# Kernel optimization log

Hardware: AMD Instinct MI355X
Metric: run time of the kernel (lower is better)

Reference implementation:

```python
import jax, jax.numpy as jnp
import numpy as np


def lstm(x, W, U, b):
    """Keras LSTM with activation='relu', recurrent_activation='sigmoid'.
    x: [B, S, E]; W: [E, 4u]; U: [u, 4u]; b: [4u]. Gate order i,f,c,o.
    Returns (all hidden states [B,S,u], last hidden [B,u])."""
    B = x.shape[0]
    u = U.shape[0]
    h0 = jnp.zeros((B, u), x.dtype)
    c0 = jnp.zeros((B, u), x.dtype)

    def step(carry, xt):
        h, c = carry
        z = xt @ W + h @ U + b
        i, f, g, o = jnp.split(z, 4, axis=-1)
        i = jax.nn.sigmoid(i)
        f = jax.nn.sigmoid(f)
        g = jax.nn.relu(g)          # candidate activation = relu
        o = jax.nn.sigmoid(o)
        c = f * c + i * g
        h = o * jax.nn.relu(c)      # output activation = relu
        return (h, c), h

    (hT, _), hs = jax.lax.scan(step, (h0, c0), jnp.swapaxes(x, 0, 1))
    return jnp.swapaxes(hs, 0, 1), hT


def setup_inputs() -> dict:
    key = jax.random.key(0)
    ks = iter(jax.random.split(key, 64))

    def W(*s):
        return jax.random.normal(next(ks), s, jnp.float32) * 0.05

    V = 32000
    inp = {
        "t": jax.random.randint(next(ks), (8, 16, 64), 0, V, jnp.int32),
        "p": jax.random.randint(next(ks), (8, 16, 512), 0, V, jnp.int32),
        "emb_t": W(V, 128),
        "emb_p": W(V, 256),
        # title LSTMs: 128 (return_seq) -> 64
        "tl0_W": W(128, 512), "tl0_U": W(128, 512), "tl0_b": jnp.zeros((512,), jnp.float32),
        "tl1_W": W(128, 256), "tl1_U": W(64, 256),  "tl1_b": jnp.zeros((256,), jnp.float32),
        # title dense: 128 relu, 64 relu, 32 linear
        "td0_W": W(64, 128),  "td0_b": jnp.zeros((128,), jnp.float32),
        "td1_W": W(128, 64),  "td1_b": jnp.zeros((64,), jnp.float32),
        "td2_W": W(64, 32),   "td2_b": jnp.zeros((32,), jnp.float32),
        # parag LSTMs: 256 (rs) -> 128 (rs) -> 64
        "pl0_W": W(256, 1024), "pl0_U": W(256, 1024), "pl0_b": jnp.zeros((1024,), jnp.float32),
        "pl1_W": W(256, 512),  "pl1_U": W(128, 512),  "pl1_b": jnp.zeros((512,), jnp.float32),
        "pl2_W": W(128, 256),  "pl2_U": W(64, 256),   "pl2_b": jnp.zeros((256,), jnp.float32),
        # parag dense: 128 relu, 64 relu, 32 linear
        "pd0_W": W(64, 128),  "pd0_b": jnp.zeros((128,), jnp.float32),
        "pd1_W": W(128, 64),  "pd1_b": jnp.zeros((64,), jnp.float32),
        "pd2_W": W(64, 32),   "pd2_b": jnp.zeros((32,), jnp.float32),
        # head: 256 relu, 128 relu, 64 relu, 32 sigmoid
        "L0_W": W(64, 256),  "L0_b": jnp.zeros((256,), jnp.float32),
        "L1_W": W(256, 128), "L1_b": jnp.zeros((128,), jnp.float32),
        "L2_W": W(128, 64),  "L2_b": jnp.zeros((64,), jnp.float32),
        "L3_W": W(64, 32),   "L3_b": jnp.zeros((32,), jnp.float32),
    }
    return inp


def reference(t, p, emb_t, emb_p,
              tl0_W, tl0_U, tl0_b, tl1_W, tl1_U, tl1_b,
              td0_W, td0_b, td1_W, td1_b, td2_W, td2_b,
              pl0_W, pl0_U, pl0_b, pl1_W, pl1_U, pl1_b, pl2_W, pl2_U, pl2_b,
              pd0_W, pd0_b, pd1_W, pd1_b, pd2_W, pd2_b,
              L0_W, L0_b, L1_W, L1_b, L2_W, L2_b, L3_W, L3_b):
    B, N, St = t.shape
    Sp = p.shape[2]

    # The original loops over B and map_fn over a singleton axis; the math is
    # identical to running the stacks on a flattened [B*N] recurrent batch.
    xt = emb_t[t.reshape(B * N, St)]              # [BN, St, 128]
    xt, _ = lstm(xt, tl0_W, tl0_U, tl0_b)         # [BN, St, 128]
    _, ht = lstm(xt, tl1_W, tl1_U, tl1_b)         # [BN, 64]
    ht = jax.nn.relu(ht @ td0_W + td0_b)
    ht = jax.nn.relu(ht @ td1_W + td1_b)
    ht = ht @ td2_W + td2_b                       # [BN, 32] (no activation)

    xp = emb_p[p.reshape(B * N, Sp)]              # [BN, Sp, 256]
    xp, _ = lstm(xp, pl0_W, pl0_U, pl0_b)
    xp, _ = lstm(xp, pl1_W, pl1_U, pl1_b)
    _, hp = lstm(xp, pl2_W, pl2_U, pl2_b)         # [BN, 64]
    hp = jax.nn.relu(hp @ pd0_W + pd0_b)
    hp = jax.nn.relu(hp @ pd1_W + pd1_b)
    hp = hp @ pd2_W + pd2_b                       # [BN, 32]

    feat = jnp.concatenate([ht, hp], axis=-1).reshape(B, N, 64)
    x = feat.mean(axis=1)                         # reduce_mean over axis=-2 (N)
    x = jax.nn.relu(x @ L0_W + L0_b)
    x = jax.nn.relu(x @ L1_W + L1_b)
    x = jax.nn.relu(x @ L2_W + L2_b)
    x = jax.nn.sigmoid(x @ L3_W + L3_b)           # [B, 32]
    return x
```

## Files before the change

### kernel.cpp

```cpp
#include <hip/hip_runtime.h>
#include <hip/hip_fp16.h>

typedef _Float16 f16;
typedef _Float16 f16x8 __attribute__((ext_vector_type(8)));
typedef float    f32x4 __attribute__((ext_vector_type(4)));
typedef unsigned short ushort;
typedef unsigned int uint;
typedef unsigned long long u64;

__device__ __forceinline__ float sigm(float x) { return 1.f / (1.f + __expf(-x)); }
__device__ __forceinline__ float reluf(float x) { return x > 0.f ? x : 0.f; }
__device__ __forceinline__ float h2f(ushort u) { return (float)__builtin_bit_cast(f16, u); }
__device__ __forceinline__ ushort f2h(float v) { return __builtin_bit_cast(ushort, (f16)v); }

#define LDRLX(p)    __hip_atomic_load((p), __ATOMIC_RELAXED, __HIP_MEMORY_SCOPE_AGENT)
#define STRLX(p, v) __hip_atomic_store((p), (v), __ATOMIC_RELAXED, __HIP_MEMORY_SCOPE_AGENT)
#define MFMA16(a, b, c) __builtin_amdgcn_mfma_f32_16x16x32_f16((a), (b), (c), 0, 0, 0)
#define LBAR() do { asm volatile("s_waitcnt lgkmcnt(0)" ::: "memory"); \
                    __builtin_amdgcn_s_barrier(); } while (0)

__device__ __forceinline__ void poll_all(uint* p, uint need, bool act) {
  bool done = !act;
  while (true) {
    if (!done) done = (LDRLX(p) >= need);
// ... 35 lines not shown
  if (id >= total) return;
  int j  = id & 7;
  int L  = (id >> 3) & 63;
  int r  = id >> 9;
  int kf = r & (KF - 1);
  int c  = r / KF;
  int k  = kf * 32 + ((L >> 4) * 8) + j;
  int n  = c * 16 + (L & 15);
  dst[id] = (f16)B[k * N + n];
}

template <int Sx, int K, int KF, int N, int NC, int MODE>
__global__ __launch_bounds__(256) void gemm_xw(const int* __restrict__ tok,
                                               const float* __restrict__ emb,
                                               const f16* __restrict__ Bsw,
                                               const float* __restrict__ bias,
                                               f16* __restrict__ X) {
  __shared__ int tokLds[64];
  __shared__ f16x8 bLds[8 * 64];
  const int tid = threadIdx.x;
  const int blk = blockIdx.x;
  const int g  = (MODE == 0) ? (blk >> 7) : (blk >> 4);
  const int t0 = (MODE == 0) ? ((blk & 127) * 4) : ((blk & 15) * 4);
  if (tid < 64) {
    int wv = tid >> 4, rho = tid & 15;
    tokLds[tid] = tok[(g * 16 + rho) * Sx + t0 + wv];
  }
  __syncthreads();
  const int wave = tid >> 6, lane = tid & 63;
  const int quad = lane >> 4, l16 = lane & 15;

  f16x8 a[KF];
  {
    const float* arow = emb + (long)tokLds[wave * 16 + l16] * K + quad * 8;
#pragma unroll
    for (int kf = 0; kf < KF; kf++) {
      float4 v0 = *(const float4*)(arow + kf * 32);
      float4 v1 = *(const float4*)(arow + kf * 32 + 4);
      f16x8 tv;
      tv[0] = (f16)v0.x; tv[1] = (f16)v0.y; tv[2] = (f16)v0.z; tv[3] = (f16)v0.w;
      tv[4] = (f16)v1.x; tv[5] = (f16)v1.y; tv[6] = (f16)v1.z; tv[7] = (f16)v1.w;
      a[kf] = tv;
    }
  }
  const int t = t0 + wave;
  const f16x8* Bfrag = (const f16x8*)Bsw;
  for (int c = 0; c < NC; c++) {
    for (int i = tid; i < KF * 64; i += 256) bLds[i] = Bfrag[c * KF * 64 + i];
    __syncthreads();
    f32x4 acc = {0.f, 0.f, 0.f, 0.f};
#pragma unroll
    for (int kf = 0; kf < KF; kf++)
      acc = MFMA16(a[kf], bLds[kf * 64 + lane], acc);
    const int col = c * 16 + l16;
    const float bc = bias[col];
    uint2 pk;
    pk.x = (uint)f2h(acc[0] + bc) | ((uint)f2h(acc[1] + bc) << 16);
    pk.y = (uint)f2h(acc[2] + bc) | ((uint)f2h(acc[3] + bc) << 16);
    size_t base;
    if (MODE == 0) {
      int gm = col >> 8, u = col & 255;
      base = (((size_t)(g * 512 + t) * 4 + gm) * 4096) + u * 16 + quad * 4;
    } else {
      int gm = col >> 7, u = col & 127;
      base = (((size_t)(g * 64 + t) * 4 + gm) * 2048) + u * 16 + quad * 4;
    }
    *(uint2*)(X + base) = pk;
    __syncthreads();
  }
}

struct RP {
  const f16 *xp2, *xt2;
  const f16 *U0f, *W1f, *U1f, *W2f, *U2f, *U0tf, *W1tf, *U1tf;
  const float *pl1_b, *pl2_b, *tl1_b;
  const float *pd0W, *pd0b, *pd1W, *pd1b, *pd2W, *pd2b;
  const float *td0W, *td0b, *td1W, *td1b, *td2W, *td2b;
  u64 *h0r, *h1r, *h0tr;
  uint *cnt;
  float* feat;
};

__global__ __launch_bounds__(256, 1) void recur_pipe(RP A) {
  __shared__ __align__(16) char smem[147968];
  const int tid = threadIdx.x;
  const int w = tid >> 6, lane = tid & 63;
  const int quad = lane >> 4, l16 = lane & 15;
  const int blk = blockIdx.x;
  const int role = blk >> 3, g = blk & 7;
  uint* mytag = A.cnt + (role * 8 + g) * 16;

  if (role < 4) {
    const int bb = role;
    f16* wlds = (f16*)smem;
    f16* hb   = (f16*)(smem + 131072);
    {
      const uint4* U0q = (const uint4*)A.U0f;
      uint4* wq = (uint4*)wlds;
      for (int idx = tid; idx < 8192; idx += 256) {
        int gm = idx >> 11, r = idx & 2047, wv = r >> 9, kf = (r >> 6) & 7, ln = r & 63;
        wq[idx] = U0q[((gm * 16 + 4 * bb + wv) * 8 + kf) * 64 + ln];
      }
    }
    for (int idx = tid; idx < 4224; idx += 256) hb[idx] = (f16)0.f;
    float c0[4] = {0.f, 0.f, 0.f, 0.f};
    u64* ringg = A.h0r + (size_t)g * 16384;
    int pp[3]; { int q = 0; for (int p = 0; p < 4; p++) if (p != bb) pp[q++] = p; }
    const uint2* xq2 = (const uint2*)A.xp2;
    const f16x8* wv8 = (const f16x8*)wlds;
    const int myu = 64 * bb + 16 * w + l16;
    const int ulq = 16 * ((tid >> 4) & 3) + (tid & 15);
    const int qd  = tid >> 6;
    uint* bpp = A.cnt;
    if (lane < 4) bpp = A.cnt + ((4 + lane) * 8 + g) * 16;
    __syncthreads();

    for (int t = 0; t < 512; t++) {
      uint2 xv[4];
      {
        size_t xb = ((size_t)(g * 512 + t) * 4) * 1024 + (size_t)myu * 4 + quad;
#pragma unroll
        for (int gm = 0; gm < 4; gm++) xv[gm] = xq2[xb + (size_t)gm * 1024];
      }
      {
        bool act = (lane < 4) && (t > 0) && ((t & 3) == 0);
        uint need = t > 4 ? (uint)(t - 4) : 0u;
        poll_all(bpp, need, act);
      }
      {
        const u64* slotb = ringg + (size_t)((t + 7) & 7) * 2048;
        const u64* ra[6]; uint nd[6]; u64 rv[6];
#pragma unroll
        for (int q = 0; q < 3; q++) {
          const u64* rb = slotb + pp[q] * 512 + 2 * tid;
          ra[q * 2] = rb; ra[q * 2 + 1] = rb + 1;
          nd[q * 2] = nd[q * 2 + 1] = (t > 0) ? (uint)t : 0u;
        }
        poll_recs<6>(ra, nd, rv);
        if (t > 0) {
          f16* dst = hb + (t & 1) * 4224;
#pragma unroll
          for (int q = 0; q < 3; q++)
#pragma unroll
            for (int j = 0; j < 2; j++) {
              uint pay = (uint)rv[q * 2 + j];
              int r0 = qd * 4 + 2 * j;
              dst[r0 * 264 + pp[q] * 64 + ulq]       = __builtin_bit_cast(f16, (ushort)pay);
              dst[(r0 + 1) * 264 + pp[q] * 64 + ulq] = __builtin_bit_cast(f16, (ushort)(pay >> 16));
            }
        }
      }
      LBAR();
      f16x8 af[8];
#pragma unroll
      for (int kf = 0; kf < 8; kf++)
        af[kf] = *(const f16x8*)&hb[(t & 1) * 4224 + l16 * 264 + kf * 32 + quad * 8];
      f32x4 z[4];
#pragma unroll
      for (int gm = 0; gm < 4; gm++) {
        f32x4 zz = {0.f, 0.f, 0.f, 0.f};
#pragma unroll
        for (int kf = 0; kf < 8; kf++)
          zz = MFMA16(af[kf], wv8[((gm * 4 + w) * 8 + kf) * 64 + lane], zz);
        z[gm] = zz;
      }
      u64 xs[4];
#pragma unroll
      for (int gm = 0; gm < 4; gm++) xs[gm] = ((u64)xv[gm].y << 32) | xv[gm].x;
      ushort hs[4];
      f16* wbuf = hb + ((t + 1) & 1) * 4224;
#pragma unroll
      for (int r = 0; r < 4; r++) {
        float gi = sigm(z[0][r] + h2f((ushort)(xs[0] >> (16 * r))));
        float ff = sigm(z[1][r] + h2f((ushort)(xs[1] >> (16 * r))));
        float gg = reluf(z[2][r] + h2f((ushort)(xs[2] >> (16 * r))));
        float oo = sigm(z[3][r] + h2f((ushort)(xs[3] >> (16 * r))));
        c0[r] = ff * c0[r] + gi * gg;
        hs[r] = f2h(oo * reluf(c0[r]));
        wbuf[(quad * 4 + r) * 264 + myu] = __builtin_bit_cast(f16, hs[r]);
      }
      {
        u64 tg = ((u64)(uint)(t + 1)) << 32;
        u64* wb = ringg + (size_t)(t & 7) * 2048 + bb * 512 +
                  quad * 128 + w * 32 + l16 * 2;
        str64(wb,     tg | (u64)((uint)hs[0] | ((uint)hs[1] << 16)));
        str64(wb + 1, tg | (u64)((uint)hs[2] | ((uint)hs[3] << 16)));
      }
    }
  } else if (role < 8) {
    const int bn = role - 4;
    f16* wlds = (f16*)smem;
    f16* h0c  = (f16*)(smem + 98304);
    f16* h1b  = (f16*)(smem + 106752);
    float* zL = (float*)(smem + 115456);
    {
      const uint4* W1q = (const uint4*)A.W1f;
      const uint4* U1q = (const uint4*)A.U1f;
      uint4* wq = (uint4*)wlds;
      for (int idx = tid; idx < 4096; idx += 256) {
        int gm = idx >> 10, r = idx & 1023, j2 = r >> 9, kf = (r >> 6) & 7, ln = r & 63;
        wq[idx] = W1q[((gm * 8 + bn * 2 + j2) * 8 + kf) * 64 + ln];
      }
      for (int idx = tid; idx < 2048; idx += 256) {
        int gm = idx >> 9, r = idx & 511, j2 = r >> 8, kf = (r >> 6) & 3, ln = r & 63;
        wq[4096 + idx] = U1q[((gm * 8 + bn * 2 + j2) * 4 + kf) * 64 + ln];
      }
    }
    for (int idx = tid; idx < 2176; idx += 256) h1b[idx] = (f16)0.f;
    float c1[2] = {0.f, 0.f};
    float bth[4];
    { int un = tid & 31; for (int gm = 0; gm < 4; gm++) bth[gm] = A.pl1_b[gm * 128 + 32 * bn + un]; }
    u64* h0rg = A.h0r + (size_t)g * 16384;
    u64* h1rg = A.h1r + (size_t)g * 8192;
    int pp[3]; { int q = 0; for (int p = 0; p < 4; p++) if (p != bn) pp[q++] = p; }
    const f16x8* wv8 = (const f16x8*)wlds;
    uint* bpp = A.cnt + (8 * 8 + g) * 16;
    __syncthreads();

    for (int t = 0; t < 512; t++) {
      {
        bool act = (lane == 0) && ((t & 3) == 0);
        uint need = t > 4 ? (uint)(t - 4) : 0u;
        poll_all(bpp, need, act);
      }
      const u64* ra[11]; uint nd[11]; u64 rv[11];
      {
        const u64* s0b = h0rg + (size_t)(t & 7) * 2048;
#pragma unroll
        for (int e = 0; e < 8; e++) { ra[e] = s0b + tid + 256 * e; nd[e] = (uint)(t + 1); }
        const u64* s1b = h1rg + (size_t)((t + 7) & 7) * 1024;
#pragma unroll
        for (int q = 0; q < 3; q++) { ra[8 + q] = s1b + pp[q] * 256 + tid; nd[8 + q] = (t > 0) ? (uint)t : 0u; }
      }
      poll_recs<11>(ra, nd, rv);
      {
#pragma unroll
        for (int e = 0; e < 8; e++) {
          int idx = tid + 256 * e;
          int bbq = idx >> 9, r = idx & 511;
          int jj = r & 1, l16c = (r >> 1) & 15, wc = (r >> 5) & 3, qdc = (r >> 7) & 3;
          int col = bbq * 64 + 16 * wc + l16c;
          int r0 = qdc * 4 + 2 * jj;
          uint pay = (uint)rv[e];
          h0c[r0 * 264 + col]       = __builtin_bit_cast(f16, (ushort)pay);
          h0c[(r0 + 1) * 264 + col] = __builtin_bit_cast(f16, (ushort)(pay >> 16));
        }
        if (t > 0) {
          f16* dst = h1b + (t & 1) * 2176;
          int sqc = tid >> 5, unc = tid & 31;
#pragma unroll
          for (int q = 0; q < 3; q++) {
            uint pay = (uint)rv[8 + q];
            dst[sqc * 136 + pp[q] * 32 + unc]       = __builtin_bit_cast(f16, (ushort)pay);
            dst[(sqc + 8) * 136 + pp[q] * 32 + unc] = __builtin_bit_cast(f16, (ushort)(pay >> 16));
          }
        }
      }
      LBAR();
      if (tid == 0) STRLX(mytag, (uint)(t + 1));
      f16x8 af0[8], af1[4];
#pragma unroll
      for (int kf = 0; kf < 8; kf++)
        af0[kf] = *(const f16x8*)&h0c[l16 * 264 + kf * 32 + quad * 8];
#pragma unroll
      for (int kf = 0; kf < 4; kf++)
        af1[kf] = *(const f16x8*)&h1b[(t & 1) * 2176 + l16 * 136 + kf * 32 + quad * 8];
#pragma unroll
      for (int j2 = 0; j2 < 2; j2++) {
        f32x4 zz = {0.f, 0.f, 0.f, 0.f};
#pragma unroll
        for (int kf = 0; kf < 8; kf++)
          zz = MFMA16(af0[kf], wv8[((w * 2 + j2) * 8 + kf) * 64 + lane], zz);
#pragma unroll
        for (int kf = 0; kf < 4; kf++)
          zz = MFMA16(af1[kf], wv8[4096 + ((w * 2 + j2) * 4 + kf) * 64 + lane], zz);
#pragma unroll
        for (int r = 0; r < 4; r++)
          zL[(quad * 4 + r) * 132 + w * 32 + j2 * 16 + l16] = zz[r];
      }
      LBAR();
      {
        int sq = tid >> 5, un = tid & 31;
        f16* dst = h1b + ((t + 1) & 1) * 2176;
        ushort hh[2];
#pragma unroll
        for (int e = 0; e < 2; e++) {
          int s = sq + 8 * e;
          float gi = sigm(zL[s * 132 + un] + bth[0]);
          float ff = sigm(zL[s * 132 + 32 + un] + bth[1]);
          float gg = reluf(zL[s * 132 + 64 + un] + bth[2]);
          float oo = sigm(zL[s * 132 + 96 + un] + bth[3]);
          c1[e] = ff * c1[e] + gi * gg;
          float hv = oo * reluf(c1[e]);
          hh[e] = f2h(hv);
          dst[s * 136 + 32 * bn + un] = __builtin_bit_cast(f16, hh[e]);
        }
        u64 tg = ((u64)(uint)(t + 1)) << 32;
        str64(h1rg + (size_t)(t & 7) * 1024 + bn * 256 + tid,
              tg | (u64)((uint)hh[0] | ((uint)hh[1] << 16)));
      }
      LBAR();
    }
  } else if (role == 8) {
    f16* wlds = (f16*)smem;
    f16* h1c  = (f16*)(smem + 98304);
    f16* h2db = (f16*)(smem + 107008);
    {
      const uint4* W2q = (const uint4*)A.W2f;
      const uint4* U2q = (const uint4*)A.U2f;
      uint4* wq = (uint4*)wlds;
      for (int idx = tid; idx < 4096; idx += 256) wq[idx] = W2q[idx];
      for (int idx = tid; idx < 2048; idx += 256) wq[4096 + idx] = U2q[idx];
    }
    for (int idx = tid; idx < 1152; idx += 256) h2db[idx] = (f16)0.f;
    float c2[4] = {0.f, 0.f, 0.f, 0.f};
    float b2[4];
#pragma unroll
    for (int gm = 0; gm < 4; gm++) b2[gm] = A.pl2_b[gm * 64 + 16 * w + l16];
    u64* h1rg = A.h1r + (size_t)g * 8192;
    const f16x8* wv8 = (const f16x8*)wlds;
    __syncthreads();

    for (int t = 0; t < 512; t++) {
      const u64* ra[4]; uint nd[4]; u64 rv[4];
      {
        const u64* s1b = h1rg + (size_t)(t & 7) * 1024;
#pragma unroll
        for (int e = 0; e < 4; e++) { ra[e] = s1b + tid + 256 * e; nd[e] = (uint)(t + 1); }
      }
      poll_recs<4>(ra, nd, rv);
      {
        f16* dst = h1c + (t & 1) * 2176;
#pragma unroll
        for (int e = 0; e < 4; e++) {
          int idx = tid + 256 * e;
          int bq = idx >> 8, r = idx & 255;
          int sqc = r >> 5, unc = r & 31;
          uint pay = (uint)rv[e];
          dst[sqc * 136 + bq * 32 + unc]       = __builtin_bit_cast(f16, (ushort)pay);
          dst[(sqc + 8) * 136 + bq * 32 + unc] = __builtin_bit_cast(f16, (ushort)(pay >> 16));
        }
      }
      LBAR();
      if (tid == 0) STRLX(mytag, (uint)(t + 1));
      f16x8 af0[4], af1[2];
#pragma unroll
      for (int kf = 0; kf < 4; kf++)
        af0[kf] = *(const f16x8*)&h1c[(t & 1) * 2176 + l16 * 136 + kf * 32 + quad * 8];
#pragma unroll
      for (int kf = 0; kf < 2; kf++)
        af1[kf] = *(const f16x8*)&h2db[(t & 1) * 1152 + l16 * 72 + kf * 32 + quad * 8];
      f32x4 z[4];
#pragma unroll
      for (int gm = 0; gm < 4; gm++) {
        f32x4 zz = {0.f, 0.f, 0.f, 0.f};
#pragma unroll
        for (int kf = 0; kf < 4; kf++)
          zz = MFMA16(af0[kf], wv8[((gm * 4 + w) * 4 + kf) * 64 + lane], zz);
#pragma unroll
        for (int kf = 0; kf < 2; kf++)
          zz = MFMA16(af1[kf], wv8[4096 + ((gm * 4 + w) * 2 + kf) * 64 + lane], zz);
        z[gm] = zz;
      }
#pragma unroll
      for (int r = 0; r < 4; r++) {
        float gi = sigm(z[0][r] + b2[0]);
        float ff = sigm(z[1][r] + b2[1]);
        float gg = reluf(z[2][r] + b2[2]);
        float oo = sigm(z[3][r] + b2[3]);
        c2[r] = ff * c2[r] + gi * gg;
        h2db[((t + 1) & 1) * 1152 + (quad * 4 + r) * 72 + 16 * w + l16] = (f16)(oo * reluf(c2[r]));
      }
    }
    __syncthreads();
    float* zmA = (float*)smem;
    float* zmB = (float*)(smem + 8448);
    const f16* hf = h2db;
#pragma unroll 1
    for (int e = 0; e < 8; e++) {
      const int idx = tid + 256 * e, sq = idx >> 7, j = idx & 127;
      float a = A.pd0b[j];
      for (int k = 0; k < 64; k++) a += (float)hf[sq * 72 + k] * A.pd0W[k * 128 + j];
      zmA[sq * 132 + j] = reluf(a);
    }
    __syncthreads();
#pragma unroll 1
    for (int e = 0; e < 4; e++) {
      const int idx = tid + 256 * e, sq = idx >> 6, j = idx & 63;
      float a = A.pd1b[j];
      for (int k = 0; k < 128; k++) a += zmA[sq * 132 + k] * A.pd1W[k * 64 + j];
      zmB[sq * 68 + j] = reluf(a);
    }
    __syncthreads();
#pragma unroll 1
    for (int e = 0; e < 2; e++) {
      const int idx = tid + 256 * e, sq = idx >> 5, j = idx & 31;
      float a = A.pd2b[j];
      for (int k = 0; k < 64; k++) a += zmB[sq * 68 + k] * A.pd2W[k * 32 + j];
      A.feat[(g * 16 + sq) * 64 + 32 + j] = a;
    }
  } else if (role < 11) {
    const int bb = role - 9;
    f16* wlds = (f16*)smem;
    f16* hb   = (f16*)(smem + 65536);
    {
      const uint4* U0tq = (const uint4*)A.U0tf;
      uint4* wq = (uint4*)wlds;
      for (int idx = tid; idx < 4096; idx += 256) {
        int gm = idx >> 10, r = idx & 1023, wv = r >> 8, kf = (r >> 6) & 3, ln = r & 63;
        wq[idx] = U0tq[((gm * 8 + 4 * bb + wv) * 4 + kf) * 64 + ln];
      }
    }
    for (int idx = tid; idx < 2176; idx += 256) hb[idx] = (f16)0.f;
    float c0[4] = {0.f, 0.f, 0.f, 0.f};
    u64* ringg = A.h0tr + (size_t)g * 8192;
    const uint2* xq2 = (const uint2*)A.xt2;
    const f16x8* wv8 = (const f16x8*)wlds;
    const int myu = 64 * bb + 16 * w + l16;
    const int pbb = bb ^ 1;
    uint* bpp = A.cnt + (11 * 8 + g) * 16;
    __syncthreads();

    for (int t = 0; t < 64; t++) {
      uint2 xv[4];
      {
        size_t xb = ((size_t)(g * 64 + t) * 4) * 512 + (size_t)myu * 4 + quad;
#pragma unroll
        for (int gm = 0; gm < 4; gm++) xv[gm] = xq2[xb + (size_t)gm * 512];
      }
      {
        bool act = (lane == 0) && (t > 0) && ((t & 3) == 0);
        uint need = t > 4 ? (uint)(t - 4) : 0u;
        poll_all(bpp, need, act);
      }
      {
        const u64* ra[2]; uint nd[2]; u64 rv[2];
        const u64* rb = ringg + (size_t)((t + 7) & 7) * 1024 + pbb * 512 + 2 * tid;
        ra[0] = rb; ra[1] = rb + 1;
        nd[0] = nd[1] = (t > 0) ? (uint)t : 0u;
        poll_recs<2>(ra, nd, rv);
        if (t > 0) {
          f16* dst = hb + (t & 1) * 2176;
          const int ul = tid >> 2;
#pragma unroll
          for (int j = 0; j < 2; j++) {
            uint pay = (uint)rv[j];
            int r0 = ((tid & 3) * 2 + j) * 2;
            dst[r0 * 136 + pbb * 64 + ul]       = __builtin_bit_cast(f16, (ushort)pay);
            dst[(r0 + 1) * 136 + pbb * 64 + ul] = __builtin_bit_cast(f16, (ushort)(pay >> 16));
          }
        }
      }
      LBAR();
      f16x8 af[4];
#pragma unroll
      for (int kf = 0; kf < 4; kf++)
        af[kf] = *(const f16x8*)&hb[(t & 1) * 2176 + l16 * 136 + kf * 32 + quad * 8];
      f32x4 z[4];
#pragma unroll
      for (int gm = 0; gm < 4; gm++) {
        f32x4 zz = {0.f, 0.f, 0.f, 0.f};
#pragma unroll
        for (int kf = 0; kf < 4; kf++)
          zz = MFMA16(af[kf], wv8[((gm * 4 + w) * 4 + kf) * 64 + lane], zz);
        z[gm] = zz;
      }
      u64 xs[4];
#pragma unroll
      for (int gm = 0; gm < 4; gm++) xs[gm] = ((u64)xv[gm].y << 32) | xv[gm].x;
      ushort hs[4];
      f16* wbuf = hb + ((t + 1) & 1) * 2176;
#pragma unroll
      for (int r = 0; r < 4; r++) {
        float gi = sigm(z[0][r] + h2f((ushort)(xs[0] >> (16 * r))));
        float ff = sigm(z[1][r] + h2f((ushort)(xs[1] >> (16 * r))));
        float gg = reluf(z[2][r] + h2f((ushort)(xs[2] >> (16 * r))));
        float oo = sigm(z[3][r] + h2f((ushort)(xs[3] >> (16 * r))));
        c0[r] = ff * c0[r] + gi * gg;
        hs[r] = f2h(oo * reluf(c0[r]));
        wbuf[(quad * 4 + r) * 136 + myu] = __builtin_bit_cast(f16, hs[r]);
      }
      {
        u64 tg = ((u64)(uint)(t + 1)) << 32;
        u64* wb = ringg + (size_t)(t & 7) * 1024 + bb * 512 + (16 * w + l16) * 8 + quad * 2;
        str64(wb,     tg | (u64)((uint)hs[0] | ((uint)hs[1] << 16)));
        str64(wb + 1, tg | (u64)((uint)hs[2] | ((uint)hs[3] << 16)));
      }
    }
  } else {
    f16* wlds = (f16*)smem;
    f16* h0tc = (f16*)(smem + 98304);
    f16* h1db = (f16*)(smem + 107008);
    {
      const uint4* W1tq = (const uint4*)A.W1tf;
      const uint4* U1tq = (const uint4*)A.U1tf;
      uint4* wq = (uint4*)wlds;
      for (int idx = tid; idx < 4096; idx += 256) wq[idx] = W1tq[idx];
      for (int idx = tid; idx < 2048; idx += 256) wq[4096 + idx] = U1tq[idx];
    }
    for (int idx = tid; idx < 1152; idx += 256) h1db[idx] = (f16)0.f;
    float c1[4] = {0.f, 0.f, 0.f, 0.f};
    float bt[4];
#pragma unroll
    for (int gm = 0; gm < 4; gm++) bt[gm] = A.tl1_b[gm * 64 + 16 * w + l16];
    u64* ringg = A.h0tr + (size_t)g * 8192;
    const f16x8* wv8 = (const f16x8*)wlds;
    __syncthreads();

    for (int t = 0; t < 64; t++) {
      const u64* ra[4]; uint nd[4]; u64 rv[4];
      {
        const u64* base = ringg + (size_t)(t & 7) * 1024;
#pragma unroll
        for (int e = 0; e < 4; e++) { ra[e] = base + tid + 256 * e; nd[e] = (uint)(t + 1); }
      }
      poll_recs<4>(ra, nd, rv);
      {
        f16* dst = h0tc + (t & 1) * 2176;
#pragma unroll
        for (int e = 0; e < 4; e++) {
          int idx = tid + 256 * e;
          int q = idx >> 9, rr = idx & 511, uls = rr >> 3, rp = rr & 7;
          uint pay = (uint)rv[e];
          dst[(2 * rp) * 136 + q * 64 + uls]     = __builtin_bit_cast(f16, (ushort)pay);
          dst[(2 * rp + 1) * 136 + q * 64 + uls] = __builtin_bit_cast(f16, (ushort)(pay >> 16));
        }
      }
      LBAR();
      if (tid == 0) STRLX(mytag, (uint)(t + 1));
      f16x8 af0[4], af1[2];
#pragma unroll
      for (int kf = 0; kf < 4; kf++)
        af0[kf] = *(const f16x8*)&h0tc[(t & 1) * 2176 + l16 * 136 + kf * 32 + quad * 8];
#pragma unroll
      for (int kf = 0; kf < 2; kf++)
        af1[kf] = *(const f16x8*)&h1db[(t & 1) * 1152 + l16 * 72 + kf * 32 + quad * 8];
      f32x4 z[4];
#pragma unroll
      for (int gm = 0; gm < 4; gm++) {
        f32x4 zz = {0.f, 0.f, 0.f, 0.f};
#pragma unroll
        for (int kf = 0; kf < 4; kf++)
          zz = MFMA16(af0[kf], wv8[((gm * 4 + w) * 4 + kf) * 64 + lane], zz);
#pragma unroll
        for (int kf = 0; kf < 2; kf++)
          zz = MFMA16(af1[kf], wv8[4096 + ((gm * 4 + w) * 2 + kf) * 64 + lane], zz);
        z[gm] = zz;
      }
#pragma unroll
      for (int r = 0; r < 4; r++) {
        float gi = sigm(z[0][r] + bt[0]);
        float ff = sigm(z[1][r] + bt[1]);
        float gg = reluf(z[2][r] + bt[2]);
        float oo = sigm(z[3][r] + bt[3]);
        c1[r] = ff * c1[r] + gi * gg;
        h1db[((t + 1) & 1) * 1152 + (quad * 4 + r) * 72 + 16 * w + l16] = (f16)(oo * reluf(c1[r]));
      }
    }
    __syncthreads();
    float* zmA = (float*)smem;
    float* zmB = (float*)(smem + 8448);
    const f16* hf = h1db;
#pragma unroll 1
    for (int e = 0; e < 8; e++) {
      const int idx = tid + 256 * e, sq = idx >> 7, j = idx & 127;
      float a = A.td0b[j];
      for (int k = 0; k < 64; k++) a += (float)hf[sq * 72 + k] * A.td0W[k * 128 + j];
      zmA[sq * 132 + j] = reluf(a);
    }
    __syncthreads();
#pragma unroll 1
    for (int e = 0; e < 4; e++) {
      const int idx = tid + 256 * e, sq = idx >> 6, j = idx & 63;
      float a = A.td1b[j];
      for (int k = 0; k < 128; k++) a += zmA[sq * 132 + k] * A.td1W[k * 64 + j];
      zmB[sq * 68 + j] = reluf(a);
    }
    __syncthreads();
#pragma unroll 1
    for (int e = 0; e < 2; e++) {
      const int idx = tid + 256 * e, sq = idx >> 5, j = idx & 31;
      float a = A.td2b[j];
      for (int k = 0; k < 64; k++) a += zmB[sq * 68 + k] * A.td2W[k * 32 + j];
      A.feat[(g * 16 + sq) * 64 + j] = a;
    }
  }
}

__global__ __launch_bounds__(256) void head_kernel(const float* __restrict__ feat,
    const float* __restrict__ L0W, const float* __restrict__ L0b,
    const float* __restrict__ L1W, const float* __restrict__ L1b,
    const float* __restrict__ L2W, const float* __restrict__ L2b,
    const float* __restrict__ L3W, const float* __restrict__ L3b,
    float* __restrict__ out) {
  __shared__ float xb[512];
  __shared__ float y0[2048];
  __shared__ float y1[1024];
  __shared__ float y2[512];
  const int tid = threadIdx.x;
  for (int idx = tid; idx < 512; idx += 256) {
    int b = idx >> 6, d = idx & 63;
    float s = 0.f;
    for (int n = 0; n < 16; n++) s += feat[(b * 16 + n) * 64 + d];
    xb[idx] = s * (1.f / 16.f);
  }
  __syncthreads();
  for (int idx = tid; idx < 2048; idx += 256) {
    int b = idx >> 8, j = idx & 255;
// ... 40 lines not shown
  const float* td0_W = (const float*)d_in[10];
  const float* td0_b = (const float*)d_in[11];
  const float* td1_W = (const float*)d_in[12];
  const float* td1_b = (const float*)d_in[13];
  const float* td2_W = (const float*)d_in[14];
  const float* td2_b = (const float*)d_in[15];
  const float* pl0_W = (const float*)d_in[16];
  const float* pl0_U = (const float*)d_in[17];
  const float* pl0_b = (const float*)d_in[18];
  const float* pl1_W = (const float*)d_in[19];
  const float* pl1_U = (const float*)d_in[20];
  const float* pl1_b = (const float*)d_in[21];
  const float* pl2_W = (const float*)d_in[22];
  const float* pl2_U = (const float*)d_in[23];
  const float* pl2_b = (const float*)d_in[24];
  const float* pd0_W = (const float*)d_in[25];
  const float* pd0_b = (const float*)d_in[26];
  const float* pd1_W = (const float*)d_in[27];
  const float* pd1_b = (const float*)d_in[28];
  const float* pd2_W = (const float*)d_in[29];
  const float* pd2_b = (const float*)d_in[30];
  const float* L0_W  = (const float*)d_in[31];
  const float* L0_b  = (const float*)d_in[32];
  const float* L1_W  = (const float*)d_in[33];
  const float* L1_b  = (const float*)d_in[34];
  const float* L2_W  = (const float*)d_in[35];
  const float* L2_b  = (const float*)d_in[36];
  const float* L3_W  = (const float*)d_in[37];
  const float* L3_b  = (const float*)d_in[38];

  char* ws = (char*)d_ws;
  size_t off = 0;
  auto alloc = [&](size_t bytes) {
    void* ptr = ws + off;
    off += (bytes + 255) & ~(size_t)255;
    return ptr;
  };
  f16* xp2  = (f16*)alloc((size_t)8 * 512 * 4 * 4096 * 2);
  f16* xt2  = (f16*)alloc((size_t)8 * 64 * 4 * 2048 * 2);
  f16* Bp   = (f16*)alloc((size_t)256 * 1024 * 2);
  f16* Bt   = (f16*)alloc((size_t)128 * 512 * 2);
  f16* U0f  = (f16*)alloc((size_t)256 * 1024 * 2);
  f16* W1f  = (f16*)alloc((size_t)256 * 512 * 2);
  f16* U1f  = (f16*)alloc((size_t)128 * 512 * 2);
  f16* W2f  = (f16*)alloc((size_t)128 * 256 * 2);
  f16* U2f  = (f16*)alloc((size_t)64 * 256 * 2);
  f16* U0tf = (f16*)alloc((size_t)128 * 512 * 2);
  f16* W1tf = (f16*)alloc((size_t)128 * 256 * 2);
  f16* U1tf = (f16*)alloc((size_t)64 * 256 * 2);
  size_t ringoff = off;
  u64* h0r  = (u64*)alloc((size_t)8 * 16384 * 8);
  u64* h1r  = (u64*)alloc((size_t)8 * 8192 * 8);
  u64* h0tr = (u64*)alloc((size_t)8 * 8192 * 8);
  uint* cnt = (uint*)alloc((size_t)96 * 16 * 4);
  size_t ringlen = off - ringoff;
  float* feat = (float*)alloc((size_t)128 * 64 * 4);

  hipMemsetAsync(ws + ringoff, 0, ringlen, stream);

  pack_bsw<8><<<1024, 256, 0, stream>>>(pl0_W, Bp, 1024);
  pack_bsw<4><<<256, 256, 0, stream>>>(tl0_W, Bt, 512);
  pack_bsw<8><<<1024, 256, 0, stream>>>(pl0_U, U0f, 1024);
  pack_bsw<8><<<512, 256, 0, stream>>>(pl1_W, W1f, 512);
  pack_bsw<4><<<256, 256, 0, stream>>>(pl1_U, U1f, 512);
  pack_bsw<4><<<128, 256, 0, stream>>>(pl2_W, W2f, 256);
  pack_bsw<2><<<64, 256, 0, stream>>>(pl2_U, U2f, 256);
  pack_bsw<4><<<256, 256, 0, stream>>>(tl0_U, U0tf, 512);
  pack_bsw<4><<<128, 256, 0, stream>>>(tl1_W, W1tf, 256);
  pack_bsw<2><<<64, 256, 0, stream>>>(tl1_U, U1tf, 256);
  gemm_xw<512, 256, 8, 1024, 64, 0><<<1024, 256, 0, stream>>>(p_tok, emb_p, Bp, pl0_b, xp2);
  gemm_xw<64, 128, 4, 512, 32, 1><<<128, 256, 0, stream>>>(t_tok, emb_t, Bt, tl0_b, xt2);

  RP ra;
  ra.xp2 = xp2; ra.xt2 = xt2;
  ra.U0f = U0f; ra.W1f = W1f; ra.U1f = U1f; ra.W2f = W2f; ra.U2f = U2f;
  ra.U0tf = U0tf; ra.W1tf = W1tf; ra.U1tf = U1tf;
  ra.pl1_b = pl1_b; ra.pl2_b = pl2_b; ra.tl1_b = tl1_b;
  ra.pd0W = pd0_W; ra.pd0b = pd0_b; ra.pd1W = pd1_W; ra.pd1b = pd1_b;
  ra.pd2W = pd2_W; ra.pd2b = pd2_b;
  ra.td0W = td0_W; ra.td0b = td0_b; ra.td1W = td1_W; ra.td1b = td1_b;
  ra.td2W = td2_W; ra.td2b = td2_b;
  ra.h0r = h0r; ra.h1r = h1r; ra.h0tr = h0tr; ra.cnt = cnt;
  ra.feat = feat;
  recur_pipe<<<96, 256, 0, stream>>>(ra);

  head_kernel<<<1, 256, 0, stream>>>(feat, L0_W, L0_b, L1_W, L1_b, L2_W, L2_b,
                                     L3_W, L3_b, (float*)d_out);
}
```

Measured before the change: 1.455 ms.

## Halve blocks per recurrent layer and keep recurrent weights in registers

```diff
diff --git a/kernel.cpp b/kernel.cpp
--- a/kernel.cpp
+++ b/kernel.cpp
@@ -141,7 +141,7 @@
 };
 
 __global__ __launch_bounds__(256, 1) void recur_pipe(RP A) {
-  __shared__ __align__(16) char smem[147968];
+  __shared__ __align__(16) char smem[139776];
   const int tid = threadIdx.x;
   const int w = tid >> 6, lane = tid & 63;
   const int quad = lane >> 4, l16 = lane & 15;
@@ -149,64 +149,68 @@
   const int role = blk >> 3, g = blk & 7;
   uint* mytag = A.cnt + (role * 8 + g) * 16;
 
-  if (role < 4) {
-    const int bb = role;
-    f16* wlds = (f16*)smem;
-    f16* hb   = (f16*)(smem + 131072);
+  if (role < 2) {
+    const int bb = role, pbb = bb ^ 1;
+    f16x8* wl8 = (f16x8*)smem;
+    f16* hb = (f16*)(smem + 65536);
+    f16x8 wr[2][4][6];
     {
+      const f16x8* U0f8 = (const f16x8*)A.U0f;
+#pragma unroll
+      for (int ut = 0; ut < 2; ut++)
+#pragma unroll
+        for (int gm = 0; gm < 4; gm++)
+#pragma unroll
+          for (int kf = 0; kf < 6; kf++)
+            wr[ut][gm][kf] =
+                U0f8[((gm * 16 + bb * 8 + w * 2 + ut) * 8 + kf) * 64 + lane];
       const uint4* U0q = (const uint4*)A.U0f;
-      uint4* wq = (uint4*)wlds;
-      for (int idx = tid; idx < 8192; idx += 256) {
-        int gm = idx >> 11, r = idx & 2047, wv = r >> 9, kf = (r >> 6) & 7, ln = r & 63;
-        wq[idx] = U0q[((gm * 16 + 4 * bb + wv) * 8 + kf) * 64 + ln];
-      }
-    }
-    for (int idx = tid; idx < 4224; idx += 256) hb[idx] = (f16)0.f;
-    float c0[4] = {0.f, 0.f, 0.f, 0.f};
+      uint4* wq = (uint4*)wl8;
+      for (int idx = tid; idx < 4096; idx += 256) {
+        int fragid = idx >> 6, ln = idx & 63;
+        int wf = fragid >> 4, ut = (fragid >> 3) & 1, gm = (fragid >> 1) & 3,
+            kfo = fragid & 1;
+        wq[idx] = U0q[((gm * 16 + bb * 8 + wf * 2 + ut) * 8 + 6 + kfo) * 64 + ln];
+      }
+    }
+    for (int idx = tid; idx < 8448; idx += 256) hb[idx] = (f16)0.f;
+    float c0[2][4] = {};
     u64* ringg = A.h0r + (size_t)g * 16384;
-    int pp[3]; { int q = 0; for (int p = 0; p < 4; p++) if (p != bb) pp[q++] = p; }
     const uint2* xq2 = (const uint2*)A.xp2;
-    const f16x8* wv8 = (const f16x8*)wlds;
-    const int myu = 64 * bb + 16 * w + l16;
-    const int ulq = 16 * ((tid >> 4) & 3) + (tid & 15);
-    const int qd  = tid >> 6;
     uint* bpp = A.cnt;
-    if (lane < 4) bpp = A.cnt + ((4 + lane) * 8 + g) * 16;
+    if (lane < 2) bpp = A.cnt + ((2 + lane) * 8 + g) * 16;
     __syncthreads();
 
     for (int t = 0; t < 512; t++) {
-      uint2 xv[4];
+      uint2 xv[2][4];
+#pragma unroll
+      for (int ut = 0; ut < 2; ut++) {
+        const int myu = 128 * bb + 32 * w + 16 * ut + l16;
+        size_t xb = ((size_t)(g * 512 + t) * 4) * 1024 + (size_t)myu * 4 + quad;
+#pragma unroll
+        for (int gm = 0; gm < 4; gm++) xv[ut][gm] = xq2[xb + (size_t)gm * 1024];
+      }
+      poll_all(bpp, t > 4 ? (uint)(t - 4) : 0u,
+               (lane < 2) && (t > 0) && ((t & 3) == 0));
       {
-        size_t xb = ((size_t)(g * 512 + t) * 4) * 1024 + (size_t)myu * 4 + quad;
-#pragma unroll
-        for (int gm = 0; gm < 4; gm++) xv[gm] = xq2[xb + (size_t)gm * 1024];
-      }
-      {
-        bool act = (lane < 4) && (t > 0) && ((t & 3) == 0);
-        uint need = t > 4 ? (uint)(t - 4) : 0u;
-        poll_all(bpp, need, act);
-      }
-      {
-        const u64* slotb = ringg + (size_t)((t + 7) & 7) * 2048;
-        const u64* ra[6]; uint nd[6]; u64 rv[6];
-#pragma unroll
-        for (int q = 0; q < 3; q++) {
-          const u64* rb = slotb + pp[q] * 512 + 2 * tid;
-          ra[q * 2] = rb; ra[q * 2 + 1] = rb + 1;
-          nd[q * 2] = nd[q * 2 + 1] = (t > 0) ? (uint)t : 0u;
-        }
-        poll_recs<6>(ra, nd, rv);
+        const u64* slotb = ringg + (size_t)((t + 7) & 7) * 2048 + pbb * 1024;
+        const u64* ra[4]; uint nd[4]; u64 rv[4];
+#pragma unroll
+        for (int e = 0; e < 4; e++) {
+          ra[e] = slotb + tid * 4 + e;
+          nd[e] = (t > 0) ? (uint)t : 0u;
+        }
+        poll_recs<4>(ra, nd, rv);
         if (t > 0) {
           f16* dst = hb + (t & 1) * 4224;
 #pragma unroll
-          for (int q = 0; q < 3; q++)
-#pragma unroll
-            for (int j = 0; j < 2; j++) {
-              uint pay = (uint)rv[q * 2 + j];
-              int r0 = qd * 4 + 2 * j;
-              dst[r0 * 264 + pp[q] * 64 + ulq]       = __builtin_bit_cast(f16, (ushort)pay);
-              dst[(r0 + 1) * 264 + pp[q] * 64 + ulq] = __builtin_bit_cast(f16, (ushort)(pay >> 16));
-            }
+          for (int e = 0; e < 4; e++) {
+            uint pay = (uint)rv[e];
+            int col = 128 * pbb + 32 * w + 16 * (e >> 1) + l16;
+            int r0 = quad * 4 + 2 * (e & 1);
+            dst[r0 * 264 + col]       = __builtin_bit_cast(f16, (ushort)pay);
+            dst[(r0 + 1) * 264 + col] = __builtin_bit_cast(f16, (ushort)(pay >> 16));
+          }
         }
       }
       LBAR();
@@ -214,104 +218,114 @@
 #pragma unroll
       for (int kf = 0; kf < 8; kf++)
         af[kf] = *(const f16x8*)&hb[(t & 1) * 4224 + l16 * 264 + kf * 32 + quad * 8];
-      f32x4 z[4];
-#pragma unroll
-      for (int gm = 0; gm < 4; gm++) {
-        f32x4 zz = {0.f, 0.f, 0.f, 0.f};
-#pragma unroll
-        for (int kf = 0; kf < 8; kf++)
-          zz = MFMA16(af[kf], wv8[((gm * 4 + w) * 8 + kf) * 64 + lane], zz);
-        z[gm] = zz;
-      }
-      u64 xs[4];
-#pragma unroll
-      for (int gm = 0; gm < 4; gm++) xs[gm] = ((u64)xv[gm].y << 32) | xv[gm].x;
-      ushort hs[4];
+      f32x4 z[2][4];
+#pragma unroll
+      for (int ut = 0; ut < 2; ut++)
+#pragma unroll
+        for (int gm = 0; gm < 4; gm++) z[ut][gm] = (f32x4){0.f, 0.f, 0.f, 0.f};
+#pragma unroll
+      for (int kf = 0; kf < 8; kf++)
+#pragma unroll
+        for (int ut = 0; ut < 2; ut++)
+#pragma unroll
+          for (int gm = 0; gm < 4; gm++) {
+            f16x8 bf = (kf < 6)
+                ? wr[ut][gm][kf]
+                : wl8[(w * 16 + ut * 8 + gm * 2 + (kf - 6)) * 64 + lane];
+            z[ut][gm] = MFMA16(af[kf], bf, z[ut][gm]);
+          }
       f16* wbuf = hb + ((t + 1) & 1) * 4224;
-#pragma unroll
-      for (int r = 0; r < 4; r++) {
-        float gi = sigm(z[0][r] + h2f((ushort)(xs[0] >> (16 * r))));
-        float ff = sigm(z[1][r] + h2f((ushort)(xs[1] >> (16 * r))));
-        float gg = reluf(z[2][r] + h2f((ushort)(xs[2] >> (16 * r))));
-        float oo = sigm(z[3][r] + h2f((ushort)(xs[3] >> (16 * r))));
-        c0[r] = ff * c0[r] + gi * gg;
-        hs[r] = f2h(oo * reluf(c0[r]));
-        wbuf[(quad * 4 + r) * 264 + myu] = __builtin_bit_cast(f16, hs[r]);
-      }
-      {
-        u64 tg = ((u64)(uint)(t + 1)) << 32;
-        u64* wb = ringg + (size_t)(t & 7) * 2048 + bb * 512 +
-                  quad * 128 + w * 32 + l16 * 2;
+      u64 tg = ((u64)(uint)(t + 1)) << 32;
+#pragma unroll
+      for (int ut = 0; ut < 2; ut++) {
+        const int myu = 128 * bb + 32 * w + 16 * ut + l16;
+        u64 xs[4];
+#pragma unroll
+        for (int gm = 0; gm < 4; gm++)
+          xs[gm] = ((u64)xv[ut][gm].y << 32) | xv[ut][gm].x;
+        ushort hs[4];
+#pragma unroll
+        for (int r = 0; r < 4; r++) {
+          float gi = sigm(z[ut][0][r] + h2f((ushort)(xs[0] >> (16 * r))));
+          float ff = sigm(z[ut][1][r] + h2f((ushort)(xs[1] >> (16 * r))));
+          float gg = reluf(z[ut][2][r] + h2f((ushort)(xs[2] >> (16 * r))));
+          float oo = sigm(z[ut][3][r] + h2f((ushort)(xs[3] >> (16 * r))));
+          c0[ut][r] = ff * c0[ut][r] + gi * gg;
+          hs[r] = f2h(oo * reluf(c0[ut][r]));
+          wbuf[(quad * 4 + r) * 264 + myu] = __builtin_bit_cast(f16, hs[r]);
+        }
+        u64* wb = ringg + (size_t)(t & 7) * 2048 + bb * 1024 + tid * 4 + ut * 2;
         str64(wb,     tg | (u64)((uint)hs[0] | ((uint)hs[1] << 16)));
         str64(wb + 1, tg | (u64)((uint)hs[2] | ((uint)hs[3] << 16)));
       }
-    }
-  } else if (role < 8) {
-    const int bn = role - 4;
-    f16* wlds = (f16*)smem;
-    f16* h0c  = (f16*)(smem + 98304);
-    f16* h1b  = (f16*)(smem + 106752);
-    float* zL = (float*)(smem + 115456);
+      LBAR();
+    }
+  } else if (role < 4) {
+    const int bn = role - 2, pbn = bn ^ 1;
+    f16* h0c = (f16*)smem;
+    f16* h1b = (f16*)(smem + 8448);
+    f16x8 wrA[4][8], wrB[4][4];
     {
-      const uint4* W1q = (const uint4*)A.W1f;
-      const uint4* U1q = (const uint4*)A.U1f;
-      uint4* wq = (uint4*)wlds;
-      for (int idx = tid; idx < 4096; idx += 256) {
-        int gm = idx >> 10, r = idx & 1023, j2 = r >> 9, kf = (r >> 6) & 7, ln = r & 63;
-        wq[idx] = W1q[((gm * 8 + bn * 2 + j2) * 8 + kf) * 64 + ln];
-      }
-      for (int idx = tid; idx < 2048; idx += 256) {
-        int gm = idx >> 9, r = idx & 511, j2 = r >> 8, kf = (r >> 6) & 3, ln = r & 63;
-        wq[4096 + idx] = U1q[((gm * 8 + bn * 2 + j2) * 4 + kf) * 64 + ln];
-      }
-    }
-    for (int idx = tid; idx < 2176; idx += 256) h1b[idx] = (f16)0.f;
-    float c1[2] = {0.f, 0.f};
+      const f16x8* W1f8 = (const f16x8*)A.W1f;
+      const f16x8* U1f8 = (const f16x8*)A.U1f;
+#pragma unroll
+      for (int gm = 0; gm < 4; gm++) {
+#pragma unroll
+        for (int kf = 0; kf < 8; kf++)
+          wrA[gm][kf] = W1f8[((gm * 8 + bn * 4 + w) * 8 + kf) * 64 + lane];
+#pragma unroll
+        for (int kf = 0; kf < 4; kf++)
+          wrB[gm][kf] = U1f8[((gm * 8 + bn * 4 + w) * 4 + kf) * 64 + lane];
+      }
+    }
+    for (int idx = tid; idx < 4352; idx += 256) h1b[idx] = (f16)0.f;
+    float c1[4] = {};
+    const int un = (bn * 4 + w) * 16 + l16;
     float bth[4];
-    { int un = tid & 31; for (int gm = 0; gm < 4; gm++) bth[gm] = A.pl1_b[gm * 128 + 32 * bn + un]; }
+#pragma unroll
+    for (int gm = 0; gm < 4; gm++) bth[gm] = A.pl1_b[gm * 128 + un];
     u64* h0rg = A.h0r + (size_t)g * 16384;
     u64* h1rg = A.h1r + (size_t)g * 8192;
-    int pp[3]; { int q = 0; for (int p = 0; p < 4; p++) if (p != bn) pp[q++] = p; }
-    const f16x8* wv8 = (const f16x8*)wlds;
-    uint* bpp = A.cnt + (8 * 8 + g) * 16;
+    uint* bpp = A.cnt + (4 * 8 + g) * 16;
     __syncthreads();
 
     for (int t = 0; t < 512; t++) {
-      {
-        bool act = (lane == 0) && ((t & 3) == 0);
-        uint need = t > 4 ? (uint)(t - 4) : 0u;
-        poll_all(bpp, need, act);
-      }
-      const u64* ra[11]; uint nd[11]; u64 rv[11];
+      poll_all(bpp, t > 4 ? (uint)(t - 4) : 0u, (lane == 0) && ((t & 3) == 0));
+      const u64* ra[10]; uint nd[10]; u64 rv[10];
       {
         const u64* s0b = h0rg + (size_t)(t & 7) * 2048;
 #pragma unroll
         for (int e = 0; e < 8; e++) { ra[e] = s0b + tid + 256 * e; nd[e] = (uint)(t + 1); }
-        const u64* s1b = h1rg + (size_t)((t + 7) & 7) * 1024;
-#pragma unroll
-        for (int q = 0; q < 3; q++) { ra[8 + q] = s1b + pp[q] * 256 + tid; nd[8 + q] = (t > 0) ? (uint)t : 0u; }
-      }
-      poll_recs<11>(ra, nd, rv);
+        const u64* s1b = h1rg + (size_t)((t + 7) & 7) * 1024 + pbn * 512;
+#pragma unroll
+        for (int j2 = 0; j2 < 2; j2++) {
+          ra[8 + j2] = s1b + tid * 2 + j2;
+          nd[8 + j2] = (t > 0) ? (uint)t : 0u;
+        }
+      }
+      poll_recs<10>(ra, nd, rv);
       {
 #pragma unroll
         for (int e = 0; e < 8; e++) {
           int idx = tid + 256 * e;
-          int bbq = idx >> 9, r = idx & 511;
-          int jj = r & 1, l16c = (r >> 1) & 15, wc = (r >> 5) & 3, qdc = (r >> 7) & 3;
-          int col = bbq * 64 + 16 * wc + l16c;
-          int r0 = qdc * 4 + 2 * jj;
+          int bbp = idx >> 10, ib = idx & 1023;
+          int lane_lin = ib >> 2, rr = ib & 3;
+          int wp = lane_lin >> 6, lp = lane_lin & 63;
+          int col = 128 * bbp + 32 * wp + 16 * (rr >> 1) + (lp & 15);
+          int r0 = (lp >> 4) * 4 + 2 * (rr & 1);
           uint pay = (uint)rv[e];
           h0c[r0 * 264 + col]       = __builtin_bit_cast(f16, (ushort)pay);
           h0c[(r0 + 1) * 264 + col] = __builtin_bit_cast(f16, (ushort)(pay >> 16));
         }
         if (t > 0) {
           f16* dst = h1b + (t & 1) * 2176;
-          int sqc = tid >> 5, unc = tid & 31;
-#pragma unroll
-          for (int q = 0; q < 3; q++) {
-            uint pay = (uint)rv[8 + q];
-            dst[sqc * 136 + pp[q] * 32 + unc]       = __builtin_bit_cast(f16, (ushort)pay);
-            dst[(sqc + 8) * 136 + pp[q] * 32 + unc] = __builtin_bit_cast(f16, (ushort)(pay >> 16));
+          int col = 64 * pbn + 16 * w + l16;
+#pragma unroll
+          for (int j2 = 0; j2 < 2; j2++) {
+            uint pay = (uint)rv[8 + j2];
+            int r0 = quad * 4 + 2 * j2;
+            dst[r0 * 136 + col]       = __builtin_bit_cast(f16, (ushort)pay);
+            dst[(r0 + 1) * 136 + col] = __builtin_bit_cast(f16, (ushort)(pay >> 16));
           }
         }
       }
@@ -324,43 +338,38 @@
 #pragma unroll
       for (int kf = 0; kf < 4; kf++)
         af1[kf] = *(const f16x8*)&h1b[(t & 1) * 2176 + l16 * 136 + kf * 32 + quad * 8];
-#pragma unroll
-      for (int j2 = 0; j2 < 2; j2++) {
-        f32x4 zz = {0.f, 0.f, 0.f, 0.f};
-#pragma unroll
-        for (int kf = 0; kf < 8; kf++)
-          zz = MFMA16(af0[kf], wv8[((w * 2 + j2) * 8 + kf) * 64 + lane], zz);
-#pragma unroll
-        for (int kf = 0; kf < 4; kf++)
-          zz = MFMA16(af1[kf], wv8[4096 + ((w * 2 + j2) * 4 + kf) * 64 + lane], zz);
-#pragma unroll
-        for (int r = 0; r < 4; r++)
-          zL[(quad * 4 + r) * 132 + w * 32 + j2 * 16 + l16] = zz[r];
+      f32x4 z[4];
+#pragma unroll
+      for (int gm = 0; gm < 4; gm++) z[gm] = (f32x4){0.f, 0.f, 0.f, 0.f};
+#pragma unroll
+      for (int kf = 0; kf < 8; kf++)
+#pragma unroll
+        for (int gm = 0; gm < 4; gm++) z[gm] = MFMA16(af0[kf], wrA[gm][kf], z[gm]);
+#pragma unroll
+      for (int kf = 0; kf < 4; kf++)
+#pragma unroll
+        for (int gm = 0; gm < 4; gm++) z[gm] = MFMA16(af1[kf], wrB[gm][kf], z[gm]);
+      f16* h1W = h1b + ((t + 1) & 1) * 2176;
+      ushort hs[4];
+#pragma unroll
+      for (int r = 0; r < 4; r++) {
+        float gi = sigm(z[0][r] + bth[0]);
+        float ff = sigm(z[1][r] + bth[1]);
+        float gg = reluf(z[2][r] + bth[2]);
+        float oo = sigm(z[3][r] + bth[3]);
+        c1[r] = ff * c1[r] + gi * gg;
+        hs[r] = f2h(oo * reluf(c1[r]));
+        h1W[(quad * 4 + r) * 136 + un] = __builtin_bit_cast(f16, hs[r]);
+      }
+      {
+        u64 tg = ((u64)(uint)(t + 1)) << 32;
+        u64* wb = h1rg + (size_t)(t & 7) * 1024 + bn * 512 + tid * 2;
+        str64(wb,     tg | (u64)((uint)hs[0] | ((uint)hs[1] << 16)));
+        str64(wb + 1, tg | (u64)((uint)hs[2] | ((uint)hs[3] << 16)));
       }
       LBAR();
-      {
-        int sq = tid >> 5, un = tid & 31;
-        f16* dst = h1b + ((t + 1) & 1) * 2176;
-        ushort hh[2];
-#pragma unroll
-        for (int e = 0; e < 2; e++) {
-          int s = sq + 8 * e;
-          float gi = sigm(zL[s * 132 + un] + bth[0]);
-          float ff = sigm(zL[s * 132 + 32 + un] + bth[1]);
-          float gg = reluf(zL[s * 132 + 64 + un] + bth[2]);
-          float oo = sigm(zL[s * 132 + 96 + un] + bth[3]);
-          c1[e] = ff * c1[e] + gi * gg;
-          float hv = oo * reluf(c1[e]);
-          hh[e] = f2h(hv);
-          dst[s * 136 + 32 * bn + un] = __builtin_bit_cast(f16, hh[e]);
-        }
-        u64 tg = ((u64)(uint)(t + 1)) << 32;
-        str64(h1rg + (size_t)(t & 7) * 1024 + bn * 256 + tid,
-              tg | (u64)((uint)hh[0] | ((uint)hh[1] << 16)));
-      }
-      LBAR();
-    }
-  } else if (role == 8) {
+    }
+  } else if (role == 4) {
     f16* wlds = (f16*)smem;
     f16* h1c  = (f16*)(smem + 98304);
     f16* h2db = (f16*)(smem + 107008);
@@ -393,11 +402,14 @@
 #pragma unroll
         for (int e = 0; e < 4; e++) {
           int idx = tid + 256 * e;
-          int bq = idx >> 8, r = idx & 255;
-          int sqc = r >> 5, unc = r & 31;
+          int bnp = idx >> 9, ib = idx & 511;
+          int lane_lin = ib >> 1, j = ib & 1;
+          int wp = lane_lin >> 6, lp = lane_lin & 63;
+          int col = 64 * bnp + 16 * wp + (lp & 15);
+          int r0 = (lp >> 4) * 4 + 2 * j;
           uint pay = (uint)rv[e];
-          dst[sqc * 136 + bq * 32 + unc]       = __builtin_bit_cast(f16, (ushort)pay);
-          dst[(sqc + 8) * 136 + bq * 32 + unc] = __builtin_bit_cast(f16, (ushort)(pay >> 16));
+          dst[r0 * 136 + col]       = __builtin_bit_cast(f16, (ushort)pay);
+          dst[(r0 + 1) * 136 + col] = __builtin_bit_cast(f16, (ushort)(pay >> 16));
         }
       }
       LBAR();
@@ -458,93 +470,75 @@
       for (int k = 0; k < 64; k++) a += zmB[sq * 68 + k] * A.pd2W[k * 32 + j];
       A.feat[(g * 16 + sq) * 64 + 32 + j] = a;
     }
-  } else if (role < 11) {
-    const int bb = role - 9;
+  } else if (role == 5) {
     f16* wlds = (f16*)smem;
-    f16* hb   = (f16*)(smem + 65536);
+    f16* hb   = (f16*)(smem + 131072);
     {
       const uint4* U0tq = (const uint4*)A.U0tf;
       uint4* wq = (uint4*)wlds;
-      for (int idx = tid; idx < 4096; idx += 256) {
-        int gm = idx >> 10, r = idx & 1023, wv = r >> 8, kf = (r >> 6) & 3, ln = r & 63;
-        wq[idx] = U0tq[((gm * 8 + 4 * bb + wv) * 4 + kf) * 64 + ln];
-      }
-    }
-    for (int idx = tid; idx < 2176; idx += 256) hb[idx] = (f16)0.f;
-    float c0[4] = {0.f, 0.f, 0.f, 0.f};
+      for (int idx = tid; idx < 8192; idx += 256) wq[idx] = U0tq[idx];
+    }
+    for (int idx = tid; idx < 4352; idx += 256) hb[idx] = (f16)0.f;
+    float c0[2][4] = {};
     u64* ringg = A.h0tr + (size_t)g * 8192;
     const uint2* xq2 = (const uint2*)A.xt2;
     const f16x8* wv8 = (const f16x8*)wlds;
-    const int myu = 64 * bb + 16 * w + l16;
-    const int pbb = bb ^ 1;
-    uint* bpp = A.cnt + (11 * 8 + g) * 16;
+    uint* bpp = A.cnt + (6 * 8 + g) * 16;
     __syncthreads();
 
     for (int t = 0; t < 64; t++) {
-      uint2 xv[4];
-      {
+      uint2 xv[2][4];
+#pragma unroll
+      for (int ut = 0; ut < 2; ut++) {
+        const int myu = 32 * w + 16 * ut + l16;
         size_t xb = ((size_t)(g * 64 + t) * 4) * 512 + (size_t)myu * 4 + quad;
 #pragma unroll
-        for (int gm = 0; gm < 4; gm++) xv[gm] = xq2[xb + (size_t)gm * 512];
-      }
-      {
-        bool act = (lane == 0) && (t > 0) && ((t & 3) == 0);
-        uint need = t > 4 ? (uint)(t - 4) : 0u;
-        poll_all(bpp, need, act);
-      }
-      {
-        const u64* ra[2]; uint nd[2]; u64 rv[2];
-        const u64* rb = ringg + (size_t)((t + 7) & 7) * 1024 + pbb * 512 + 2 * tid;
-        ra[0] = rb; ra[1] = rb + 1;
-        nd[0] = nd[1] = (t > 0) ? (uint)t : 0u;
-        poll_recs<2>(ra, nd, rv);
-        if (t > 0) {
-          f16* dst = hb + (t & 1) * 2176;
-          const int ul = tid >> 2;
-#pragma unroll
-          for (int j = 0; j < 2; j++) {
-            uint pay = (uint)rv[j];
-            int r0 = ((tid & 3) * 2 + j) * 2;
-            dst[r0 * 136 + pbb * 64 + ul]       = __builtin_bit_cast(f16, (ushort)pay);
-            dst[(r0 + 1) * 136 + pbb * 64 + ul] = __builtin_bit_cast(f16, (ushort)(pay >> 16));
-          }
-        }
-      }
-      LBAR();
+        for (int gm = 0; gm < 4; gm++) xv[ut][gm] = xq2[xb + (size_t)gm * 512];
+      }
+      poll_all(bpp, t > 4 ? (uint)(t - 4) : 0u,
+               (lane == 0) && (t > 0) && ((t & 3) == 0));
       f16x8 af[4];
 #pragma unroll
       for (int kf = 0; kf < 4; kf++)
         af[kf] = *(const f16x8*)&hb[(t & 1) * 2176 + l16 * 136 + kf * 32 + quad * 8];
-      f32x4 z[4];
-#pragma unroll
-      for (int gm = 0; gm < 4; gm++) {
-        f32x4 zz = {0.f, 0.f, 0.f, 0.f};
-#pragma unroll
-        for (int kf = 0; kf < 4; kf++)
-          zz = MFMA16(af[kf], wv8[((gm * 4 + w) * 4 + kf) * 64 + lane], zz);
-        z[gm] = zz;
-      }
-      u64 xs[4];
-#pragma unroll
-      for (int gm = 0; gm < 4; gm++) xs[gm] = ((u64)xv[gm].y << 32) | xv[gm].x;
-      ushort hs[4];
+      f32x4 z[2][4];
+#pragma unroll
+      for (int ut = 0; ut < 2; ut++)
+#pragma unroll
+        for (int gm = 0; gm < 4; gm++) z[ut][gm] = (f32x4){0.f, 0.f, 0.f, 0.f};
+#pragma unroll
+      for (int kf = 0; kf < 4; kf++)
+#pragma unroll
+        for (int ut = 0; ut < 2; ut++)
+#pragma unroll
+          for (int gm = 0; gm < 4; gm++)
+            z[ut][gm] = MFMA16(af[kf],
+                wv8[((gm * 8 + w * 2 + ut) * 4 + kf) * 64 + lane], z[ut][gm]);
       f16* wbuf = hb + ((t + 1) & 1) * 2176;
-#pragma unroll
-      for (int r = 0; r < 4; r++) {
-        float gi = sigm(z[0][r] + h2f((ushort)(xs[0] >> (16 * r))));
-        float ff = sigm(z[1][r] + h2f((ushort)(xs[1] >> (16 * r))));
-        float gg = reluf(z[2][r] + h2f((ushort)(xs[2] >> (16 * r))));
-        float oo = sigm(z[3][r] + h2f((ushort)(xs[3] >> (16 * r))));
-        c0[r] = ff * c0[r] + gi * gg;
-        hs[r] = f2h(oo * reluf(c0[r]));
-        wbuf[(quad * 4 + r) * 136 + myu] = __builtin_bit_cast(f16, hs[r]);
-      }
-      {
-        u64 tg = ((u64)(uint)(t + 1)) << 32;
-        u64* wb = ringg + (size_t)(t & 7) * 1024 + bb * 512 + (16 * w + l16) * 8 + quad * 2;
+      u64 tg = ((u64)(uint)(t + 1)) << 32;
+#pragma unroll
+      for (int ut = 0; ut < 2; ut++) {
+        const int myu = 32 * w + 16 * ut + l16;
+        u64 xs[4];
+#pragma unroll
+        for (int gm = 0; gm < 4; gm++)
+          xs[gm] = ((u64)xv[ut][gm].y << 32) | xv[ut][gm].x;
+        ushort hs[4];
+#pragma unroll
+        for (int r = 0; r < 4; r++) {
+          float gi = sigm(z[ut][0][r] + h2f((ushort)(xs[0] >> (16 * r))));
+          float ff = sigm(z[ut][1][r] + h2f((ushort)(xs[1] >> (16 * r))));
+          float gg = reluf(z[ut][2][r] + h2f((ushort)(xs[2] >> (16 * r))));
+          float oo = sigm(z[ut][3][r] + h2f((ushort)(xs[3] >> (16 * r))));
+          c0[ut][r] = ff * c0[ut][r] + gi * gg;
+          hs[r] = f2h(oo * reluf(c0[ut][r]));
+          wbuf[(quad * 4 + r) * 136 + myu] = __builtin_bit_cast(f16, hs[r]);
+        }
+        u64* wb = ringg + (size_t)(t & 7) * 1024 + tid * 4 + ut * 2;
         str64(wb,     tg | (u64)((uint)hs[0] | ((uint)hs[1] << 16)));
         str64(wb + 1, tg | (u64)((uint)hs[2] | ((uint)hs[3] << 16)));
       }
+      LBAR();
     }
   } else {
     f16* wlds = (f16*)smem;
@@ -571,18 +565,18 @@
       {
         const u64* base = ringg + (size_t)(t & 7) * 1024;
 #pragma unroll
-        for (int e = 0; e < 4; e++) { ra[e] = base + tid + 256 * e; nd[e] = (uint)(t + 1); }
+        for (int e = 0; e < 4; e++) { ra[e] = base + tid * 4 + e; nd[e] = (uint)(t + 1); }
       }
       poll_recs<4>(ra, nd, rv);
       {
         f16* dst = h0tc + (t & 1) * 2176;
 #pragma unroll
         for (int e = 0; e < 4; e++) {
-          int idx = tid + 256 * e;
-          int q = idx >> 9, rr = idx & 511, uls = rr >> 3, rp = rr & 7;
           uint pay = (uint)rv[e];
-          dst[(2 * rp) * 136 + q * 64 + uls]     = __builtin_bit_cast(f16, (ushort)pay);
-          dst[(2 * rp + 1) * 136 + q * 64 + uls] = __builtin_bit_cast(f16, (ushort)(pay >> 16));
+          int col = 32 * w + 16 * (e >> 1) + l16;
+          int r0 = quad * 4 + 2 * (e & 1);
+          dst[r0 * 136 + col]       = __builtin_bit_cast(f16, (ushort)pay);
+          dst[(r0 + 1) * 136 + col] = __builtin_bit_cast(f16, (ushort)(pay >> 16));
         }
       }
       LBAR();
@@ -789,7 +783,7 @@
   ra.td2W = td2_W; ra.td2b = td2_b;
   ra.h0r = h0r; ra.h1r = h1r; ra.h0tr = h0tr; ra.cnt = cnt;
   ra.feat = feat;
-  recur_pipe<<<96, 256, 0, stream>>>(ra);
+  recur_pipe<<<56, 256, 0, stream>>>(ra);
 
   head_kernel<<<1, 256, 0, stream>>>(feat, L0_W, L0_b, L1_W, L1_b, L2_W, L2_b,
                                      L3_W, L3_b, (float*)d_out);
```

New measurement: 1.966 ms. +35.1%, slower.
